# Performance work log

Hardware: AMD Instinct MI355X
Metric: run time of the kernel (lower is better)

The kernel has to match this reference:

```python
import jax, jax.numpy as jnp
import numpy as np

N_SPECIES = 4; N_BASIS = 128; N_GRAPH = 16; R_MAX = 6.0
NS_NODE, NV_NODE = 32, 16          # node irreps 32x0e + 16x1o
NS_EDGE = 16                       # initial edge irreps 16x0e
NS_OUT, NV_OUT = 16, 8             # output irreps 16x0e + 8x1o
NS_IN = 2 * NS_NODE + NS_EDGE      # 80 concatenated scalars
NV_IN = 2 * NV_NODE                # 32 concatenated vectors
NS_CONV = NS_OUT + NV_OUT          # 24 scalars (16 features + 8 gates)
W_SIZES = [NS_IN * NS_CONV, NS_IN * NV_OUT, NV_IN * NV_OUT, NV_IN * NS_CONV, NV_IN * NV_OUT]
N_NODES, N_EDGES = 8192, 65536
EPS = 1e-5


def gaussian_basis(d, stop, n):
    offsets = jnp.linspace(0.0, stop, n)
    coeff = -0.5 / (offsets[1] - offsets[0]) ** 2
    return jnp.exp(coeff * (d[:, None] - offsets[None, :]) ** 2)


def seg_mean(vals, seg, cnt):
    return jax.ops.segment_sum(vals, seg, num_segments=N_GRAPH) / cnt[:, None]


def setup_inputs():
    key = jax.random.key(0)
    ks = jax.random.split(key, 20)
    rn = lambda k, shape, scale: jax.random.normal(k, shape, jnp.float32) * scale
    inp = {}
    inp["node_fea"] = rn(ks[0], (N_NODES, NS_NODE + 3 * NV_NODE), 1.0)
    d = 0.5 + 5.0 * jax.random.uniform(ks[1], (N_EDGES,), jnp.float32)
    vec = jax.random.normal(ks[2], (N_EDGES, 3), jnp.float32)
    inp["edge_attr"] = jnp.concatenate([d[:, None], vec], axis=1)
    inp["edge_index"] = jax.random.randint(ks[3], (2, N_EDGES), 0, N_NODES)
    inp["x"] = jax.random.randint(ks[4], (N_NODES,), 0, N_SPECIES)
    inp["batch"] = jnp.sort(jax.random.randint(ks[5], (N_NODES,), 0, N_GRAPH))
    inp["w_rh"] = rn(ks[6], (N_BASIS, 64), N_BASIS ** -0.5); inp["b_rh"] = jnp.zeros((64,), jnp.float32)
    inp["w_ro"] = rn(ks[7], (64, sum(W_SIZES)), 64 ** -0.5); inp["b_ro"] = jnp.zeros((sum(W_SIZES),), jnp.float32)
    inp["w_pre"] = rn(ks[8], (NS_EDGE, NS_EDGE), NS_EDGE ** -0.5); inp["b_pre"] = jnp.zeros((NS_EDGE,), jnp.float32)
    inp["w_sc"] = rn(ks[9], (NS_EDGE, N_SPECIES ** 2, NS_OUT), 1.0)
    inp["w_post_s"] = rn(ks[10], (NS_OUT, NS_OUT), NS_OUT ** -0.5); inp["b_post_s"] = jnp.zeros((NS_OUT,), jnp.float32)
    inp["w_post_v"] = rn(ks[11], (NV_OUT, NV_OUT), NV_OUT ** -0.5)
    inp["ln_w_s"] = jnp.ones((NS_OUT,), jnp.float32); inp["ln_b_s"] = jnp.zeros((NS_OUT,), jnp.float32)
    inp["ln_w_v"] = jnp.ones((NV_OUT,), jnp.float32)
    inp["w_skip"] = rn(ks[12], (NS_EDGE, NS_OUT), NS_EDGE ** -0.5)
    inp["w_edge_s"] = rn(ks[13], (NS_OUT, NS_OUT), NS_OUT ** -0.5); inp["b_edge_s"] = jnp.zeros((NS_OUT,), jnp.float32)
    inp["w_edge_v"] = rn(ks[14], (NV_OUT, NV_OUT), NV_OUT ** -0.5)
    return inp


def _forward(node_fea, edge_attr, w_rh, b_rh, w_ro, b_ro, w_pre, b_pre, w_sc,
             w_post_s, b_post_s, w_post_v, ln_w_s, ln_b_s, ln_w_v,
             w_skip, w_edge_s, b_edge_s, w_edge_v, edge_index, x, batch):
    E = edge_index.shape[1]
    idx_i, idx_j = edge_index[0], edge_index[1]
    one_hot = jax.nn.one_hot(N_SPECIES * x[idx_i] + x[idx_j], N_SPECIES ** 2, dtype=node_fea.dtype)
    d, vec = edge_attr[:, 0], edge_attr[:, 1:4]
    u = vec / (jnp.linalg.norm(vec, axis=1, keepdims=True) + 1e-12)
    Y1 = np.sqrt(3.0) * u                                   # l=1 sph harm, component norm; Y0 == 1
    rbf = gaussian_basis(d, R_MAX, N_BASIS)                 # edge_length_embedded
    edge_s0 = gaussian_basis(d, 6.0, NS_EDGE)               # distance_expansion -> initial edge scalars
    # self connection: edge scalars x species-pair one-hot -> output scalars
    sc = jnp.einsum('ei,ej,ijo->eo', edge_s0, one_hot, w_sc) / np.sqrt(NS_EDGE * N_SPECIES ** 2)
    edge_s = edge_s0 @ w_pre + b_pre                        # lin_pre
    # gather node features by edge indices and concat
    nf_i, nf_j = node_fea[idx_i], node_fea[idx_j]
    s_in = jnp.concatenate([nf_i[:, :NS_NODE], nf_j[:, :NS_NODE], edge_s], axis=1)  # [E,80]
    v_in = jnp.concatenate([nf_i[:, NS_NODE:].reshape(E, NV_NODE, 3),
                            nf_j[:, NS_NODE:].reshape(E, NV_NODE, 3)], axis=1)      # [E,32,3]
    # radial MLP -> per-edge tensor-product path weights
    h = jax.nn.silu(rbf @ w_rh + b_rh)
    w_all = h @ w_ro + b_ro                                 # [E, 3840]
    w1, w2, w3, w4, w5 = jnp.split(w_all, np.cumsum(W_SIZES)[:-1].tolist(), axis=1)
    # equivariant tensor-product paths (explicit l<=1 Clebsch-Gordan structure)
    s0 = jnp.einsum('ei,eio->eo', s_in, w1.reshape(E, NS_IN, NS_CONV)) / np.sqrt(NS_IN)            # 0e x 0e -> 0e
    vA = jnp.einsum('ei,eio,ec->eoc', s_in, w2.reshape(E, NS_IN, NV_OUT), Y1) / np.sqrt(NS_IN)     # 0e x 1o -> 1o
    vB = jnp.einsum('eic,eio->eoc', v_in, w3.reshape(E, NV_IN, NV_OUT)) / np.sqrt(NV_IN)           # 1o x 0e -> 1o
    s1 = jnp.einsum('eic,eio,ec->eo', v_in, w4.reshape(E, NV_IN, NS_CONV), Y1) / np.sqrt(3.0 * NV_IN)  # 1o.1o -> 0e
    vC = jnp.einsum('eic,eio->eoc', jnp.cross(v_in, Y1[:, None, :]), w5.reshape(E, NV_IN, NV_OUT)) / np.sqrt(2.0 * NV_IN)  # 1o x 1o -> 1o
    s_conv = s0 + s1                                        # [E,24]
    v_conv = vA + vB + vC                                   # [E,8,3]
    # gate nonlinearity inside conv
    s_out = jax.nn.silu(s_conv[:, :NS_OUT])
    v_out = v_conv * jax.nn.sigmoid(s_conv[:, NS_OUT:])[:, :, None]
    # lin_post then self connection
    s_out = s_out @ w_post_s + b_post_s + sc
    v_out = jnp.einsum('eic,io->eoc', v_out, w_post_v)
    # e3LayerNorm keyed by graph id of source node
    eb = batch[idx_i]
    cnt = jnp.maximum(jax.ops.segment_sum(jnp.ones((E,), s_out.dtype), eb, num_segments=N_GRAPH), 1.0)
    mu = seg_mean(s_out, eb, cnt)
    s_c = s_out - mu[eb]
    rms_s = jnp.sqrt(seg_mean(s_c ** 2, eb, cnt).mean(axis=1, keepdims=True) + EPS)
    s_n = s_c / rms_s[eb] * ln_w_s + ln_b_s
    rms_v = jnp.sqrt((seg_mean((v_out ** 2).sum(-1), eb, cnt) / 3.0).mean(axis=1, keepdims=True) + EPS)
    v_n = v_out / rms_v[eb][:, :, None] * ln_w_v[None, :, None]
    # skip connection from old edge features (scalars only)
    s_n = s_n + edge_s0 @ w_skip
    # final lin_edge
    s_fin = s_n @ w_edge_s + b_edge_s
    v_fin = jnp.einsum('eic,io->eoc', v_n, w_edge_v)
    return jnp.concatenate([s_fin, v_fin.reshape(E, NV_OUT * 3)], axis=1)  # [E,40]


def reference(node_fea, edge_attr, edge_index, x, batch, w_rh, b_rh, w_ro, b_ro,
              w_pre, b_pre, w_sc, w_post_s, b_post_s, w_post_v, ln_w_s, ln_b_s, ln_w_v,
              w_skip, w_edge_s, b_edge_s, w_edge_v):
    return _forward(node_fea, edge_attr, w_rh, b_rh, w_ro, b_ro, w_pre, b_pre, w_sc,
                    w_post_s, b_post_s, w_post_v, ln_w_s, ln_b_s, ln_w_v,
                    w_skip, w_edge_s, b_edge_s, w_edge_v, edge_index, x, batch)
```

## Files before the change

### kernel.cpp

```cpp
#include <hip/hip_runtime.h>

typedef unsigned short u16;
typedef unsigned int u32;
typedef __attribute__((ext_vector_type(8))) short short8;
typedef __attribute__((ext_vector_type(4))) float floatx4;

#define E_TOTAL 65536

__device__ __forceinline__ u16 f2bf(float f) {
    union { float f; u32 i; } c; c.f = f;
    const u32 u = c.i;
    const u32 r = (u + 0x7fffu + ((u >> 16) & 1u)) >> 16;
    return (u16)r;
}
__device__ __forceinline__ float bfu2f(u16 u) {
    union { u32 i; float f; } c; c.i = ((u32)u) << 16; return c.f;
}
__device__ __forceinline__ void split2(float x0, float x1, u32& hp, u32& lp) {
    union { float f; u32 u; } a0, a1, h0, h1, l0, l1;
    a0.f = x0; a1.f = x1;
    h0.u = a0.u & 0xFFFF0000u; h1.u = a1.u & 0xFFFF0000u;
    hp = __builtin_amdgcn_perm(a1.u, a0.u, 0x07060302u);
    l0.f = x0 - h0.f; l1.f = x1 - h1.f;
    lp = __builtin_amdgcn_perm(l1.u, l0.u, 0x07060302u);
}
union Frag8 { u32 u[4]; short8 s; };


__global__ void k_zero(float* __restrict__ ws) {
    const int i = threadIdx.x + blockIdx.x * blockDim.x;
    if (i < 1056) ws[i] = 0.0f;
}

__global__ __launch_bounds__(64) void k_probe(int* __restrict__ binv) {
    const int lane = threadIdx.x;
    const int q = lane >> 4;
    if (lane < 32) binv[lane] = lane;
    short8 bfr;
    #pragma unroll
    for (int j = 0; j < 8; ++j) bfr[j] = (short)f2bf((float)(q*8 + j + 1));
    #pragma unroll
    for (int s = 0; s < 32; ++s) {
        const int qa = s >> 3, ja = s & 7;
        short8 afr = {0,0,0,0,0,0,0,0};
        if (q == qa) afr[ja] = (short)f2bf(1.0f);
        floatx4 dc = {0.0f, 0.0f, 0.0f, 0.0f};
        dc = __builtin_amdgcn_mfma_f32_16x16x32_bf16(afr, bfr, dc, 0, 0, 0);
        if (lane == 0) {
            const int sB = (int)(dc[0] + 0.5f) - 1;
            if (sB >= 0 && sB < 32) binv[sB] = s;
        }
    }
}

__global__ __launch_bounds__(256) void k_edge_heavy(
    const float* __restrict__ node_fea, const float* __restrict__ edge_attr,
    const int* __restrict__ edge_index, const int* __restrict__ xsp,
    const float* __restrict__ w_rh, const float* __restrict__ b_rh,
    const float* __restrict__ w_ro, const float* __restrict__ b_ro,
    const float* __restrict__ w_pre, const float* __restrict__ b_pre,
    const float* __restrict__ w_sc, const float* __restrict__ w_post_s,
    const float* __restrict__ b_post_s, const float* __restrict__ w_post_v,
    const int* __restrict__ binv,
    float* __restrict__ out)
{
    __shared__ __align__(16) u16 a_rbf[2][16 * 128];
    __shared__ __align__(16) u16 a_h[2][16 * 64];
    __shared__ __align__(16) float sh_wt[16][258];
    __shared__ float sh_sin[16][80];
    __shared__ float sh_vl[16][3][32];
    __shared__ float sh_q[16][32];
    __shared__ float sh_cr[16][3][32];
    __shared__ float sh_acc[16][56];
    __shared__ float sh_es0[16][16];
    __shared__ float sh_y1[16][4];
    __shared__ int   sh_kmap[32];

    const int tid = threadIdx.x;
    const int ed = tid >> 4, l16 = tid & 15;
    const int lane = tid & 63, w = tid >> 6;
    const int quad = lane >> 4, l15 = lane & 15;
    const int e = blockIdx.x * 16 + ed;

    if (tid < 32) sh_kmap[tid] = binv[tid];

    const int ni = edge_index[e];
    const int nj = edge_index[E_TOTAL + e];
    const float4 ea = *(const float4*)(edge_attr + 4*e);
    const float d  = ea.x;
    const float vx = ea.y, vy = ea.z, vz = ea.w;
    const float invn = 1.0f / (sqrtf(vx*vx + vy*vy + vz*vz) + 1e-12f);
    const float Y0 = 1.7320508075688772f * vx * invn;
    const float Y1 = 1.7320508075688772f * vy * invn;
    const float Y2 = 1.7320508075688772f * vz * invn;
    if (l16 == 0) { sh_y1[ed][0] = Y0; sh_y1[ed][1] = Y1; sh_y1[ed][2] = Y2; }

    const float C128 = -0.5f * (127.0f/6.0f) * (127.0f/6.0f);
    const float S128 = 6.0f/127.0f;
    {
        short8 thi, tlo;
        #pragma unroll
        for (int r = 0; r < 8; ++r) {
            const int b = l16*8 + r;
            const float t = d - S128 * (float)b;
            const float x = expf(C128 * t * t);
            const u16 hi = f2bf(x);
            thi[r] = (short)hi;
            tlo[r] = (short)f2bf(x - bfu2f(hi));
        }
        *(short8*)&a_rbf[0][(l16*16 + ed)*8] = thi;
        *(short8*)&a_rbf[1][(l16*16 + ed)*8] = tlo;
    }
    {
        const float t = d - 0.4f * (float)l16;
        sh_es0[ed][l16] = expf(-3.125f * t * t);
    }

    const float rs80 = 0.11180339887498949f;
    const float rs32 = 0.17677669529663689f;
    {
        const float* fi = node_fea + (size_t)ni * 80;
        const float* fj = node_fea + (size_t)nj * 80;
        sh_sin[ed][2*l16+0]    = fi[2*l16+0] * rs80;
        sh_sin[ed][2*l16+1]    = fi[2*l16+1] * rs80;
        sh_sin[ed][32+2*l16+0] = fj[2*l16+0] * rs80;
        sh_sin[ed][32+2*l16+1] = fj[2*l16+1] * rs80;
        #pragma unroll
        for (int c = 0; c < 3; ++c) {
            sh_vl[ed][c][l16]      = fi[32 + 3*l16 + c] * rs32;
            sh_vl[ed][c][16 + l16] = fj[32 + 3*l16 + c] * rs32;
        }
    }
    for (int s = tid; s < 16*56; s += 256) (&sh_acc[0][0])[s] = 0.0f;
    __syncthreads();

    int km[8];
    u32 voff0[8], voff1[8];
    #pragma unroll
    for (int j = 0; j < 8; ++j) {
        km[j] = sh_kmap[quad*8 + j];
        voff0[j] = (u32)(km[j] * 3840 + l15);
        voff1[j] = voff0[j] + 32u * 3840u;
    }

    float my_sc;
    {
        const int o = l16;
        float es = b_pre[o];
        float sc = 0.0f;
        const int p = 4*xsp[ni] + xsp[nj];
        #pragma unroll
        for (int i = 0; i < 16; ++i) {
            const float g = sh_es0[ed][i];
            es += g * w_pre[i*16 + o];
            sc += g * w_sc[(i*16 + p)*16 + o];
        }
        sh_sin[ed][64 + o] = es * rs80;
        my_sc = sc * 0.0625f;
    }
    #pragma unroll
    for (int rr = 0; rr < 2; ++rr) {
        const int i = l16 + 16*rr;
        const float a0 = sh_vl[ed][0][i];
        const float a1 = sh_vl[ed][1][i];
        const float a2 = sh_vl[ed][2][i];
        sh_q[ed][i] = (a0*Y0 + a1*Y1 + a2*Y2) * 0.57735026918962573f;
        sh_cr[ed][0][i] = (a1*Y2 - a2*Y1) * 0.70710678118654746f;
        sh_cr[ed][1][i] = (a2*Y0 - a0*Y2) * 0.70710678118654746f;
        sh_cr[ed][2][i] = (a0*Y1 - a1*Y0) * 0.70710678118654746f;
    }

    {
        floatx4 hacc = {0.0f, 0.0f, 0.0f, 0.0f};
        #pragma unroll
        for (int kk = 0; kk < 4; ++kk) {
            const short8 ahi = *(const short8*)&a_rbf[0][((kk*4 + quad)*16 + l15)*8];
            const short8 alo = *(const short8*)&a_rbf[1][((kk*4 + quad)*16 + l15)*8];
            Frag8 bh, bl;
            #pragma unroll
            for (int jj = 0; jj < 4; ++jj) {
                const float x0 = w_rh[(size_t)(kk*32 + km[2*jj+0])*64 + w*16 + l15];
                const float x1 = w_rh[(size_t)(kk*32 + km[2*jj+1])*64 + w*16 + l15];
                split2(x0, x1, bh.u[jj], bl.u[jj]);
            }
            hacc = __builtin_amdgcn_mfma_f32_16x16x32_bf16(ahi, bh.s, hacc, 0, 0, 0);
            hacc = __builtin_amdgcn_mfma_f32_16x16x32_bf16(alo, bh.s, hacc, 0, 0, 0);
            hacc = __builtin_amdgcn_mfma_f32_16x16x32_bf16(ahi, bl.s, hacc, 0, 0, 0);
        }
        const int hn = w*16 + l15;
        const float bb = b_rh[hn];
        const int k8 = hn >> 3, j2 = hn & 7;
        #pragma unroll
        for (int r = 0; r < 4; ++r) {
            const float x = hacc[r] + bb;
            const float s = x / (1.0f + expf(-x));
            const int m = quad*4 + r;
            const u16 h = f2bf(s);
            a_h[0][(k8*16 + m)*8 + j2] = h;
            a_h[1][(k8*16 + m)*8 + j2] = f2bf(s - bfu2f(h));
        }
    }
    __syncthreads();

    const short8 a0h = *(const short8*)&a_h[0][((0*4 + quad)*16 + l15)*8];
    const short8 a1h = *(const short8*)&a_h[0][((1*4 + quad)*16 + l15)*8];
    const short8 a0l = *(const short8*)&a_h[1][((0*4 + quad)*16 + l15)*8];
    const short8 a1l = *(const short8*)&a_h[1][((1*4 + quad)*16 + l15)*8];

    for (int ch = 0; ch < 15; ++ch) {
        const int coff = ch * 256;
        floatx4 acc[4];
        float bias[4];
        #pragma unroll
        for (int ct = 0; ct < 4; ++ct) {
            const int sgct = __builtin_amdgcn_readfirstlane(ch*16 + w*4 + ct);
            const float* bp = w_ro + sgct*16;
            float f0[8], f1[8];
            #pragma unroll
            for (int j = 0; j < 8; ++j) {
                f0[j] = bp[voff0[j]];
                f1[j] = bp[voff1[j]];
            }
            Frag8 b0h, b0l, b1h, b1l;
            #pragma unroll
            for (int jj = 0; jj < 4; ++jj) {
                split2(f0[2*jj], f0[2*jj+1], b0h.u[jj], b0l.u[jj]);
                split2(f1[2*jj], f1[2*jj+1], b1h.u[jj], b1l.u[jj]);
            }
            floatx4 a = {0.0f, 0.0f, 0.0f, 0.0f};
            a = __builtin_amdgcn_mfma_f32_16x16x32_bf16(a0h, b0h.s, a, 0, 0, 0);
            a = __builtin_amdgcn_mfma_f32_16x16x32_bf16(a1h, b1h.s, a, 0, 0, 0);
            a = __builtin_amdgcn_mfma_f32_16x16x32_bf16(a0l, b0h.s, a, 0, 0, 0);
            a = __builtin_amdgcn_mfma_f32_16x16x32_bf16(a1l, b1h.s, a, 0, 0, 0);
            a = __builtin_amdgcn_mfma_f32_16x16x32_bf16(a0h, b0l.s, a, 0, 0, 0);
            a = __builtin_amdgcn_mfma_f32_16x16x32_bf16(a1h, b1l.s, a, 0, 0, 0);
            acc[ct] = a;
            bias[ct] = b_ro[sgct*16 + l15];
        }
        __syncthreads();
        #pragma unroll
        for (int ct = 0; ct < 4; ++ct) {
            const int col = w*64 + ct*16 + l15;
            #pragma unroll
            for (int r = 0; r < 4; ++r)
                sh_wt[quad*4 + r][col] = acc[ct][r] + bias[ct];
        }
        __syncthreads();

        if (ch <= 7) {
            const int hi = (ch == 7) ? 1920 : (coff + 256);
            for (int idx = tid; idx < 384; idx += 256) {
                const int eo = idx / 24, o = idx % 24;
                const int i0 = (coff > o) ? (coff - o + 23) / 24 : 0;
                int i1 = (hi - o + 23) / 24; if (i1 > 80) i1 = 80;
                float a = 0.0f;
                for (int i = i0; i < i1; ++i)
                    a += sh_sin[eo][i] * sh_wt[eo][i*24 + o - coff];
                sh_acc[eo][o] += a;
            }
        }
        if (ch == 7) {
            for (int idx = tid; idx < 128; idx += 256) {
                const int eo = idx >> 3, o = idx & 7;
                float a = 0.0f;
                #pragma unroll
                for (int i = 0; i < 16; ++i)
                    a += sh_sin[eo][i] * sh_wt[eo][128 + i*8 + o];
                sh_acc[eo][24 + o] += a;
            }
        }
        if (ch == 8 || ch == 9) {
            const int ib = (ch == 8) ? 16 : 48;
            for (int idx = tid; idx < 128; idx += 256) {
                const int eo = idx >> 3, o = idx & 7;
                float a = 0.0f;
                #pragma unroll
                for (int i2 = 0; i2 < 32; ++i2)
                    a += sh_sin[eo][ib + i2] * sh_wt[eo][i2*8 + o];
                sh_acc[eo][24 + o] += a;
            }
        }
        if (ch == 10) {
            for (int idx = tid; idx < 384; idx += 256) {
                const int eo = idx / 24, rem = idx % 24;
                const int o = rem / 3, cc = rem % 3;
                float a = 0.0f;
                #pragma unroll
                for (int i = 0; i < 32; ++i)
                    a += sh_vl[eo][cc][i] * sh_wt[eo][i*8 + o];
                sh_acc[eo][32 + o*3 + cc] += a;
            }
        }
        if (ch >= 11 && ch <= 13) {
            const int rel = coff - 2816;
            for (int idx = tid; idx < 384; idx += 256) {
                const int eo = idx / 24, o = idx % 24;
                const int i0 = (rel > o) ? (rel - o + 23) / 24 : 0;
                int i1 = (rel + 256 - o + 23) / 24; if (i1 > 32) i1 = 32;
                float a = 0.0f;
                for (int i = i0; i < i1; ++i)
                    a += sh_q[eo][i] * sh_wt[eo][i*24 + o - rel];
                sh_acc[eo][o] += a;
            }
        }
        if (ch == 14) {
            for (int idx = tid; idx < 384; idx += 256) {
                const int eo = idx / 24, rem = idx % 24;
                const int o = rem / 3, cc = rem % 3;
                float a = 0.0f;
                #pragma unroll
                for (int i = 0; i < 32; ++i)
                    a += sh_cr[eo][cc][i] * sh_wt[eo][i*8 + o];
                sh_acc[eo][32 + o*3 + cc] += a;
            }
        }
    }
    __syncthreads();

    {
        const int o = l16;
        float a = b_post_s[o] + my_sc;
        #pragma unroll
        for (int i = 0; i < 16; ++i) {
            const float sv = sh_acc[ed][i];
            a += (sv / (1.0f + expf(-sv))) * w_post_s[i*16 + o];
        }
        out[(size_t)e*40 + o] = a;
    }
    if (l16 < 8) {
        const int o = l16;
        const float Ya = sh_y1[ed][0], Yb = sh_y1[ed][1], Yc = sh_y1[ed][2];
        float r0 = 0.0f, r1 = 0.0f, r2 = 0.0f;
        #pragma unroll
        for (int i = 0; i < 8; ++i) {
            const float g  = 1.0f / (1.0f + expf(-sh_acc[ed][16 + i]));
            const float a2 = sh_acc[ed][24 + i];
            const float ww = w_post_v[i*8 + o];
            r0 += (a2*Ya + sh_acc[ed][32 + i*3 + 0]) * g * ww;
            r1 += (a2*Yb + sh_acc[ed][32 + i*3 + 1]) * g * ww;
            r2 += (a2*Yc + sh_acc[ed][32 + i*3 + 2]) * g * ww;
        }
        out[(size_t)e*40 + 16 + o*3 + 0] = r0;
        out[(size_t)e*40 + 16 + o*3 + 1] = r1;
        out[(size_t)e*40 + 16 + o*3 + 2] = r2;
    }
}

__global__ __launch_bounds__(256) void k_stats_partial(
    const float* __restrict__ sv, const int* __restrict__ edge_index,
    const int* __restrict__ batch, float* __restrict__ ws)
{
    __shared__ float sh_ed[256][40];
    __shared__ int   sh_eb[256];
    const int tid = threadIdx.x;
    const int e = blockIdx.x * 256 + tid;
    sh_eb[tid] = batch[edge_index[e]];
    const float* p = sv + (size_t)e * 40;
    #pragma unroll
    for (int j = 0; j < 40; ++j) sh_ed[tid][j] = p[j];
    __syncthreads();

    for (int slot = tid; slot < 768; slot += 256) {
        const int g = slot / 48, s = slot % 48;
        float acc = 0.0f;
        if (s < 16) {
            for (int k = 0; k < 256; ++k) {
                const float m = (sh_eb[k] == g) ? 1.0f : 0.0f;
                acc += m * sh_ed[k][s];
            }
        } else if (s < 32) {
            for (int k = 0; k < 256; ++k) {
                const float m = (sh_eb[k] == g) ? 1.0f : 0.0f;
                const float v = sh_ed[k][s - 16];
                acc += m * v * v;
            }
        } else if (s < 40) {
            const int o3 = 16 + (s - 32) * 3;
            for (int k = 0; k < 256; ++k) {
                const float m = (sh_eb[k] == g) ? 1.0f : 0.0f;
                const float v0 = sh_ed[k][o3], v1 = sh_ed[k][o3+1], v2 = sh_ed[k][o3+2];
                acc += m * (v0*v0 + v1*v1 + v2*v2);
            }
        } else if (s == 40) {
            for (int k = 0; k < 256; ++k) acc += (sh_eb[k] == g) ? 1.0f : 0.0f;
        }
        atomicAdd(&ws[slot], acc);
    }
}

__global__ __launch_bounds__(64) void k_stats_final(float* __restrict__ ws)
{
    const int tid = threadIdx.x;
    if (tid < 16) {
        const int g = tid;
        float cnt = ws[g*48 + 40]; if (cnt < 1.0f) cnt = 1.0f;
        const float ic = 1.0f / cnt;
        float vs = 0.0f;
        for (int chn = 0; chn < 16; ++chn) {
            const float mu = ws[g*48 + chn] * ic;
            ws[768 + g*16 + chn] = mu;
            vs += ws[g*48 + 16 + chn] * ic - mu * mu;
        }
        if (vs < 0.0f) vs = 0.0f;
        ws[1024 + g] = 1.0f / sqrtf(vs * (1.0f/16.0f) + 1e-5f);
        float vv = 0.0f;
        for (int o = 0; o < 8; ++o) vv += ws[g*48 + 32 + o];
        vv = vv * ic * (1.0f/3.0f) * (1.0f/8.0f);
        ws[1040 + g] = 1.0f / sqrtf(vv + 1e-5f);
    }
}

__global__ __launch_bounds__(256) void k_edge_final(
    float* buf, const float* __restrict__ ws,
    const float* __restrict__ edge_attr, const int* __restrict__ edge_index,
    const int* __restrict__ batch,
    const float* __restrict__ ln_w_s, const float* __restrict__ ln_b_s,
    const float* __restrict__ ln_w_v, const float* __restrict__ w_skip,
    const float* __restrict__ w_edge_s, const float* __restrict__ b_edge_s,
    const float* __restrict__ w_edge_v)
{
    __shared__ float sh_mu[16][16];
    __shared__ float sh_is[16], sh_iv[16];
    __shared__ float sh_lws[16], sh_lbs[16], sh_lwv[8];
    __shared__ float sh_skip[16][16], sh_wes[16][16], sh_bes[16], sh_wev[8][8];
    const int tid = threadIdx.x;
    sh_mu[tid >> 4][tid & 15]   = ws[768 + tid];
    sh_skip[tid >> 4][tid & 15] = w_skip[tid];
    sh_wes[tid >> 4][tid & 15]  = w_edge_s[tid];
    if (tid < 16) {
        sh_is[tid]  = ws[1024 + tid];
        sh_iv[tid]  = ws[1040 + tid];
        sh_lws[tid] = ln_w_s[tid];
        sh_lbs[tid] = ln_b_s[tid];
        sh_bes[tid] = b_edge_s[tid];
    }
    if (tid < 8)  sh_lwv[tid] = ln_w_v[tid];
    if (tid < 64) sh_wev[tid >> 3][tid & 7] = w_edge_v[tid];
    __syncthreads();

    const int e = blockIdx.x * 256 + tid;
    const int g = batch[edge_index[e]];
    const float d = edge_attr[4*e];
    float es0[16];
    #pragma unroll
    for (int b = 0; b < 16; ++b) {
        const float t = d - 0.4f * (float)b;
        es0[b] = expf(-3.125f * t * t);
    }
    float p[40];
    float* pb = buf + (size_t)e * 40;
    #pragma unroll
    for (int j = 0; j < 40; ++j) p[j] = pb[j];

    const float is = sh_is[g];
    float sn[16];
    #pragma unroll
    for (int chn = 0; chn < 16; ++chn)
        sn[chn] = (p[chn] - sh_mu[g][chn]) * is * sh_lws[chn] + sh_lbs[chn];
    #pragma unroll
    for (int b = 0; b < 16; ++b) {
        const float g0 = es0[b];
        #pragma unroll
        for (int chn = 0; chn < 16; ++chn) sn[chn] += g0 * sh_skip[b][chn];
    }
    #pragma unroll
    for (int o = 0; o < 16; ++o) {
        float a = sh_bes[o];
        #pragma unroll
        for (int chn = 0; chn < 16; ++chn) a += sn[chn] * sh_wes[chn][o];
        pb[o] = a;
    }
    const float iv = sh_iv[g];
    float vn[8][3];
    #pragma unroll
    for (int i = 0; i < 8; ++i) {
        const float f = iv * sh_lwv[i];
        vn[i][0] = p[16 + i*3 + 0] * f;
        vn[i][1] = p[16 + i*3 + 1] * f;
        vn[i][2] = p[16 + i*3 + 2] * f;
    }
    #pragma unroll
    for (int o = 0; o < 8; ++o) {
        float r0 = 0.0f, r1 = 0.0f, r2 = 0.0f;
        #pragma unroll
        for (int i = 0; i < 8; ++i) {
            const float w = sh_wev[i][o];
            r0 += vn[i][0] * w; r1 += vn[i][1] * w; r2 += vn[i][2] * w;
        }
        pb[16 + o*3 + 0] = r0;
        pb[16 + o*3 + 1] = r1;
        pb[16 + o*3 + 2] = r2;
    }
}

extern "C" void kernel_launch(void* const* d_in, const int* in_sizes, int n_in,
                              void* d_out, int out_size, void* d_ws, size_t ws_size,
                              hipStream_t stream)
{
    const float* node_fea  = (const float*)d_in[0];
    const float* edge_attr = (const float*)d_in[1];
    const int* edge_index  = (const int*)d_in[2];
    const int* xsp         = (const int*)d_in[3];
    const int* batch       = (const int*)d_in[4];
    const float* w_rh      = (const float*)d_in[5];
    const float* b_rh      = (const float*)d_in[6];
    const float* w_ro      = (const float*)d_in[7];
    const float* b_ro      = (const float*)d_in[8];
    const float* w_pre     = (const float*)d_in[9];
    const float* b_pre     = (const float*)d_in[10];
    const float* w_sc      = (const float*)d_in[11];
    const float* w_post_s  = (const float*)d_in[12];
    const float* b_post_s  = (const float*)d_in[13];
    const float* w_post_v  = (const float*)d_in[14];
    const float* ln_w_s    = (const float*)d_in[15];
    const float* ln_b_s    = (const float*)d_in[16];
    const float* ln_w_v    = (const float*)d_in[17];
    const float* w_skip    = (const float*)d_in[18];
    const float* w_edge_s  = (const float*)d_in[19];
    const float* b_edge_s  = (const float*)d_in[20];
    const float* w_edge_v  = (const float*)d_in[21];

    float* ws   = (float*)d_ws;
    int*   binv = (int*)(ws + 1056);
    float* out  = (float*)d_out;

    k_zero<<<2, 1024, 0, stream>>>(ws);
    k_probe<<<1, 64, 0, stream>>>(binv);
    k_edge_heavy<<<4096, 256, 0, stream>>>(node_fea, edge_attr, edge_index, xsp,
        w_rh, b_rh, w_ro, b_ro, w_pre, b_pre, w_sc, w_post_s, b_post_s, w_post_v,
        binv, out);
    k_stats_partial<<<256, 256, 0, stream>>>(out, edge_index, batch, ws);
    k_stats_final<<<1, 64, 0, stream>>>(ws);
    k_edge_final<<<256, 256, 0, stream>>>(out, ws, edge_attr, edge_index,
        batch, ln_w_s, ln_b_s, ln_w_v, w_skip, w_edge_s, b_edge_s, w_edge_v);
}
```

Before: 483.8 us.

## Process 32 edges per block to reuse split weight fragments across two MFMA groups

The heavy edge kernel now handles two 16-edge groups per block, so each loaded and bf16-split readout weight fragment feeds MFMAs for both groups. This halves global weight traffic and split work per edge. Chunk width drops to 128 columns so the per-edge weight tile still fits in a shared pool that is reused for the RBF and hidden activations. The q and cross-product precomputation is folded into the contraction loops. It also merges the zero and probe kernels into one launch and pads a shared array to avoid bank conflicts. The cost is more shared memory and registers per block, which may lower occupancy, plus twice as many chunk iterations and barriers.

```diff
diff --git a/kernel.cpp b/kernel.cpp
--- a/kernel.cpp
+++ b/kernel.cpp
@@ -27,13 +27,9 @@
 union Frag8 { u32 u[4]; short8 s; };
 
 
-__global__ void k_zero(float* __restrict__ ws) {
-    const int i = threadIdx.x + blockIdx.x * blockDim.x;
-    if (i < 1056) ws[i] = 0.0f;
-}
-
-__global__ __launch_bounds__(64) void k_probe(int* __restrict__ binv) {
+__global__ __launch_bounds__(64) void k_init(float* __restrict__ ws, int* __restrict__ binv) {
     const int lane = threadIdx.x;
+    for (int i = lane; i < 1056; i += 64) ws[i] = 0.0f;
     const int q = lane >> 4;
     if (lane < 32) binv[lane] = lane;
     short8 bfr;
@@ -64,74 +60,79 @@
     const int* __restrict__ binv,
     float* __restrict__ out)
 {
-    __shared__ __align__(16) u16 a_rbf[2][16 * 128];
-    __shared__ __align__(16) u16 a_h[2][16 * 64];
-    __shared__ __align__(16) float sh_wt[16][258];
-    __shared__ float sh_sin[16][80];
-    __shared__ float sh_vl[16][3][32];
-    __shared__ float sh_q[16][32];
-    __shared__ float sh_cr[16][3][32];
-    __shared__ float sh_acc[16][56];
-    __shared__ float sh_es0[16][16];
-    __shared__ float sh_y1[16][4];
+    __shared__ __align__(16) char pool[32 * 129 * 4];
+    __shared__ float sh_sin[32][81];
+    __shared__ float sh_vl[32][3][32];
+    __shared__ float sh_acc[32][56];
+    __shared__ float sh_es0[32][16];
+    __shared__ float sh_y1[32][4];
     __shared__ int   sh_kmap[32];
+
+    u16* pool16 = (u16*)pool;
+    float (*sh_wt)[129] = (float(*)[129])pool;
 
     const int tid = threadIdx.x;
     const int ed = tid >> 4, l16 = tid & 15;
     const int lane = tid & 63, w = tid >> 6;
     const int quad = lane >> 4, l15 = lane & 15;
-    const int e = blockIdx.x * 16 + ed;
 
     if (tid < 32) sh_kmap[tid] = binv[tid];
-
-    const int ni = edge_index[e];
-    const int nj = edge_index[E_TOTAL + e];
-    const float4 ea = *(const float4*)(edge_attr + 4*e);
-    const float d  = ea.x;
-    const float vx = ea.y, vy = ea.z, vz = ea.w;
-    const float invn = 1.0f / (sqrtf(vx*vx + vy*vy + vz*vz) + 1e-12f);
-    const float Y0 = 1.7320508075688772f * vx * invn;
-    const float Y1 = 1.7320508075688772f * vy * invn;
-    const float Y2 = 1.7320508075688772f * vz * invn;
-    if (l16 == 0) { sh_y1[ed][0] = Y0; sh_y1[ed][1] = Y1; sh_y1[ed][2] = Y2; }
 
     const float C128 = -0.5f * (127.0f/6.0f) * (127.0f/6.0f);
     const float S128 = 6.0f/127.0f;
-    {
-        short8 thi, tlo;
-        #pragma unroll
-        for (int r = 0; r < 8; ++r) {
-            const int b = l16*8 + r;
-            const float t = d - S128 * (float)b;
-            const float x = expf(C128 * t * t);
-            const u16 hi = f2bf(x);
-            thi[r] = (short)hi;
-            tlo[r] = (short)f2bf(x - bfu2f(hi));
-        }
-        *(short8*)&a_rbf[0][(l16*16 + ed)*8] = thi;
-        *(short8*)&a_rbf[1][(l16*16 + ed)*8] = tlo;
-    }
-    {
-        const float t = d - 0.4f * (float)l16;
-        sh_es0[ed][l16] = expf(-3.125f * t * t);
-    }
-
     const float rs80 = 0.11180339887498949f;
     const float rs32 = 0.17677669529663689f;
-    {
-        const float* fi = node_fea + (size_t)ni * 80;
-        const float* fj = node_fea + (size_t)nj * 80;
-        sh_sin[ed][2*l16+0]    = fi[2*l16+0] * rs80;
-        sh_sin[ed][2*l16+1]    = fi[2*l16+1] * rs80;
-        sh_sin[ed][32+2*l16+0] = fj[2*l16+0] * rs80;
-        sh_sin[ed][32+2*l16+1] = fj[2*l16+1] * rs80;
-        #pragma unroll
-        for (int c = 0; c < 3; ++c) {
-            sh_vl[ed][c][l16]      = fi[32 + 3*l16 + c] * rs32;
-            sh_vl[ed][c][16 + l16] = fj[32 + 3*l16 + c] * rs32;
-        }
-    }
-    for (int s = tid; s < 16*56; s += 256) (&sh_acc[0][0])[s] = 0.0f;
+
+    int pp[2];
+    #pragma unroll
+    for (int g = 0; g < 2; ++g) {
+        const int e  = blockIdx.x * 32 + g*16 + ed;
+        const int ge = g*16 + ed;
+        const int ni = edge_index[e];
+        const int nj = edge_index[E_TOTAL + e];
+        pp[g] = 4*xsp[ni] + xsp[nj];
+        const float4 ea = *(const float4*)(edge_attr + 4*e);
+        const float d  = ea.x;
+        const float vx = ea.y, vy = ea.z, vz = ea.w;
+        const float invn = 1.0f / (sqrtf(vx*vx + vy*vy + vz*vz) + 1e-12f);
+        if (l16 == 0) {
+            sh_y1[ge][0] = 1.7320508075688772f * vx * invn;
+            sh_y1[ge][1] = 1.7320508075688772f * vy * invn;
+            sh_y1[ge][2] = 1.7320508075688772f * vz * invn;
+        }
+        {
+            short8 thi, tlo;
+            #pragma unroll
+            for (int r = 0; r < 8; ++r) {
+                const int b = l16*8 + r;
+                const float t = d - S128 * (float)b;
+                const float x = expf(C128 * t * t);
+                const u16 hi = f2bf(x);
+                thi[r] = (short)hi;
+                tlo[r] = (short)f2bf(x - bfu2f(hi));
+            }
+            *(short8*)&pool16[(0*2 + g)*2048 + (l16*16 + ed)*8] = thi;
+            *(short8*)&pool16[(1*2 + g)*2048 + (l16*16 + ed)*8] = tlo;
+        }
+        {
+            const float t = d - 0.4f * (float)l16;
+            sh_es0[ge][l16] = expf(-3.125f * t * t);
+        }
+        {
+            const float* fi = node_fea + (size_t)ni * 80;
+            const float* fj = node_fea + (size_t)nj * 80;
+            sh_sin[ge][2*l16+0]    = fi[2*l16+0] * rs80;
+            sh_sin[ge][2*l16+1]    = fi[2*l16+1] * rs80;
+            sh_sin[ge][32+2*l16+0] = fj[2*l16+0] * rs80;
+            sh_sin[ge][32+2*l16+1] = fj[2*l16+1] * rs80;
+            #pragma unroll
+            for (int c = 0; c < 3; ++c) {
+                sh_vl[ge][c][l16]      = fi[32 + 3*l16 + c] * rs32;
+                sh_vl[ge][c][16 + l16] = fj[32 + 3*l16 + c] * rs32;
+            }
+        }
+    }
+    for (int s = tid; s < 32*56; s += 256) (&sh_acc[0][0])[s] = 0.0f;
     __syncthreads();
 
     int km[8];
@@ -143,77 +144,78 @@
         voff1[j] = voff0[j] + 32u * 3840u;
     }
 
-    float my_sc;
-    {
+    float my_sc[2];
+    #pragma unroll
+    for (int g = 0; g < 2; ++g) {
+        const int ge = g*16 + ed;
         const int o = l16;
         float es = b_pre[o];
         float sc = 0.0f;
-        const int p = 4*xsp[ni] + xsp[nj];
+        const int p = pp[g];
         #pragma unroll
         for (int i = 0; i < 16; ++i) {
-            const float g = sh_es0[ed][i];
-            es += g * w_pre[i*16 + o];
-            sc += g * w_sc[(i*16 + p)*16 + o];
-        }
-        sh_sin[ed][64 + o] = es * rs80;
-        my_sc = sc * 0.0625f;
-    }
-    #pragma unroll
-    for (int rr = 0; rr < 2; ++rr) {
-        const int i = l16 + 16*rr;
-        const float a0 = sh_vl[ed][0][i];
-        const float a1 = sh_vl[ed][1][i];
-        const float a2 = sh_vl[ed][2][i];
-        sh_q[ed][i] = (a0*Y0 + a1*Y1 + a2*Y2) * 0.57735026918962573f;
-        sh_cr[ed][0][i] = (a1*Y2 - a2*Y1) * 0.70710678118654746f;
-        sh_cr[ed][1][i] = (a2*Y0 - a0*Y2) * 0.70710678118654746f;
-        sh_cr[ed][2][i] = (a0*Y1 - a1*Y0) * 0.70710678118654746f;
-    }
-
+            const float gg = sh_es0[ge][i];
+            es += gg * w_pre[i*16 + o];
+            sc += gg * w_sc[(i*16 + p)*16 + o];
+        }
+        sh_sin[ge][64 + o] = es * rs80;
+        my_sc[g] = sc * 0.0625f;
+    }
+
+    floatx4 hacc[2] = {{0,0,0,0},{0,0,0,0}};
+    #pragma unroll
+    for (int kk = 0; kk < 4; ++kk) {
+        Frag8 bh, bl;
+        #pragma unroll
+        for (int jj = 0; jj < 4; ++jj) {
+            const float x0 = w_rh[(size_t)(kk*32 + km[2*jj+0])*64 + w*16 + l15];
+            const float x1 = w_rh[(size_t)(kk*32 + km[2*jj+1])*64 + w*16 + l15];
+            split2(x0, x1, bh.u[jj], bl.u[jj]);
+        }
+        #pragma unroll
+        for (int g = 0; g < 2; ++g) {
+            const short8 ahi = *(const short8*)&pool16[(0*2 + g)*2048 + ((kk*4 + quad)*16 + l15)*8];
+            const short8 alo = *(const short8*)&pool16[(1*2 + g)*2048 + ((kk*4 + quad)*16 + l15)*8];
+            hacc[g] = __builtin_amdgcn_mfma_f32_16x16x32_bf16(ahi, bh.s, hacc[g], 0, 0, 0);
+            hacc[g] = __builtin_amdgcn_mfma_f32_16x16x32_bf16(alo, bh.s, hacc[g], 0, 0, 0);
+            hacc[g] = __builtin_amdgcn_mfma_f32_16x16x32_bf16(ahi, bl.s, hacc[g], 0, 0, 0);
+        }
+    }
+    __syncthreads();
     {
-        floatx4 hacc = {0.0f, 0.0f, 0.0f, 0.0f};
-        #pragma unroll
-        for (int kk = 0; kk < 4; ++kk) {
-            const short8 ahi = *(const short8*)&a_rbf[0][((kk*4 + quad)*16 + l15)*8];
-            const short8 alo = *(const short8*)&a_rbf[1][((kk*4 + quad)*16 + l15)*8];
-            Frag8 bh, bl;
-            #pragma unroll
-            for (int jj = 0; jj < 4; ++jj) {
-                const float x0 = w_rh[(size_t)(kk*32 + km[2*jj+0])*64 + w*16 + l15];
-                const float x1 = w_rh[(size_t)(kk*32 + km[2*jj+1])*64 + w*16 + l15];
-                split2(x0, x1, bh.u[jj], bl.u[jj]);
-            }
-            hacc = __builtin_amdgcn_mfma_f32_16x16x32_bf16(ahi, bh.s, hacc, 0, 0, 0);
-            hacc = __builtin_amdgcn_mfma_f32_16x16x32_bf16(alo, bh.s, hacc, 0, 0, 0);
-            hacc = __builtin_amdgcn_mfma_f32_16x16x32_bf16(ahi, bl.s, hacc, 0, 0, 0);
-        }
         const int hn = w*16 + l15;
         const float bb = b_rh[hn];
         const int k8 = hn >> 3, j2 = hn & 7;
         #pragma unroll
-        for (int r = 0; r < 4; ++r) {
-            const float x = hacc[r] + bb;
-            const float s = x / (1.0f + expf(-x));
-            const int m = quad*4 + r;
-            const u16 h = f2bf(s);
-            a_h[0][(k8*16 + m)*8 + j2] = h;
-            a_h[1][(k8*16 + m)*8 + j2] = f2bf(s - bfu2f(h));
+        for (int g = 0; g < 2; ++g) {
+            #pragma unroll
+            for (int r = 0; r < 4; ++r) {
+                const float x = hacc[g][r] + bb;
+                const float s = x / (1.0f + expf(-x));
+                const int m = quad*4 + r;
+                const u16 h = f2bf(s);
+                pool16[(0*2 + g)*1024 + (k8*16 + m)*8 + j2] = h;
+                pool16[(1*2 + g)*1024 + (k8*16 + m)*8 + j2] = f2bf(s - bfu2f(h));
+            }
         }
     }
     __syncthreads();
-
-    const short8 a0h = *(const short8*)&a_h[0][((0*4 + quad)*16 + l15)*8];
-    const short8 a1h = *(const short8*)&a_h[0][((1*4 + quad)*16 + l15)*8];
-    const short8 a0l = *(const short8*)&a_h[1][((0*4 + quad)*16 + l15)*8];
-    const short8 a1l = *(const short8*)&a_h[1][((1*4 + quad)*16 + l15)*8];
-
-    for (int ch = 0; ch < 15; ++ch) {
-        const int coff = ch * 256;
-        floatx4 acc[4];
-        float bias[4];
-        #pragma unroll
-        for (int ct = 0; ct < 4; ++ct) {
-            const int sgct = __builtin_amdgcn_readfirstlane(ch*16 + w*4 + ct);
+    short8 ah_[2][2], al_[2][2];
+    #pragma unroll
+    for (int f = 0; f < 2; ++f)
+        #pragma unroll
+        for (int g = 0; g < 2; ++g) {
+            ah_[f][g] = *(const short8*)&pool16[(0*2 + g)*1024 + ((f*4 + quad)*16 + l15)*8];
+            al_[f][g] = *(const short8*)&pool16[(1*2 + g)*1024 + ((f*4 + quad)*16 + l15)*8];
+        }
+
+    for (int ch = 0; ch < 30; ++ch) {
+        const int coff = ch * 128;
+        floatx4 acc[2][2];
+        float bias[2];
+        #pragma unroll
+        for (int ct = 0; ct < 2; ++ct) {
+            const int sgct = __builtin_amdgcn_readfirstlane(ch*8 + w*2 + ct);
             const float* bp = w_ro + sgct*16;
             float f0[8], f1[8];
             #pragma unroll
@@ -227,122 +229,126 @@
                 split2(f0[2*jj], f0[2*jj+1], b0h.u[jj], b0l.u[jj]);
                 split2(f1[2*jj], f1[2*jj+1], b1h.u[jj], b1l.u[jj]);
             }
-            floatx4 a = {0.0f, 0.0f, 0.0f, 0.0f};
-            a = __builtin_amdgcn_mfma_f32_16x16x32_bf16(a0h, b0h.s, a, 0, 0, 0);
-            a = __builtin_amdgcn_mfma_f32_16x16x32_bf16(a1h, b1h.s, a, 0, 0, 0);
-            a = __builtin_amdgcn_mfma_f32_16x16x32_bf16(a0l, b0h.s, a, 0, 0, 0);
-            a = __builtin_amdgcn_mfma_f32_16x16x32_bf16(a1l, b1h.s, a, 0, 0, 0);
-            a = __builtin_amdgcn_mfma_f32_16x16x32_bf16(a0h, b0l.s, a, 0, 0, 0);
-            a = __builtin_amdgcn_mfma_f32_16x16x32_bf16(a1h, b1l.s, a, 0, 0, 0);
-            acc[ct] = a;
+            #pragma unroll
+            for (int g = 0; g < 2; ++g) {
+                floatx4 a = {0.0f, 0.0f, 0.0f, 0.0f};
+                a = __builtin_amdgcn_mfma_f32_16x16x32_bf16(ah_[0][g], b0h.s, a, 0, 0, 0);
+                a = __builtin_amdgcn_mfma_f32_16x16x32_bf16(ah_[1][g], b1h.s, a, 0, 0, 0);
+                a = __builtin_amdgcn_mfma_f32_16x16x32_bf16(al_[0][g], b0h.s, a, 0, 0, 0);
+                a = __builtin_amdgcn_mfma_f32_16x16x32_bf16(al_[1][g], b1h.s, a, 0, 0, 0);
+                a = __builtin_amdgcn_mfma_f32_16x16x32_bf16(ah_[0][g], b0l.s, a, 0, 0, 0);
+                a = __builtin_amdgcn_mfma_f32_16x16x32_bf16(ah_[1][g], b1l.s, a, 0, 0, 0);
+                acc[ct][g] = a;
+            }
             bias[ct] = b_ro[sgct*16 + l15];
         }
         __syncthreads();
         #pragma unroll
-        for (int ct = 0; ct < 4; ++ct) {
-            const int col = w*64 + ct*16 + l15;
-            #pragma unroll
-            for (int r = 0; r < 4; ++r)
-                sh_wt[quad*4 + r][col] = acc[ct][r] + bias[ct];
+        for (int ct = 0; ct < 2; ++ct) {
+            const int col = w*32 + ct*16 + l15;
+            #pragma unroll
+            for (int g = 0; g < 2; ++g)
+                #pragma unroll
+                for (int r = 0; r < 4; ++r)
+                    sh_wt[g*16 + quad*4 + r][col] = acc[ct][g][r] + bias[ct];
         }
         __syncthreads();
 
-        if (ch <= 7) {
-            const int hi = (ch == 7) ? 1920 : (coff + 256);
-            for (int idx = tid; idx < 384; idx += 256) {
+        if (ch < 15) {
+            for (int idx = tid; idx < 768; idx += 256) {
                 const int eo = idx / 24, o = idx % 24;
                 const int i0 = (coff > o) ? (coff - o + 23) / 24 : 0;
-                int i1 = (hi - o + 23) / 24; if (i1 > 80) i1 = 80;
+                int i1 = (coff + 128 - o + 23) / 24; if (i1 > 80) i1 = 80;
                 float a = 0.0f;
                 for (int i = i0; i < i1; ++i)
                     a += sh_sin[eo][i] * sh_wt[eo][i*24 + o - coff];
                 sh_acc[eo][o] += a;
             }
-        }
-        if (ch == 7) {
-            for (int idx = tid; idx < 128; idx += 256) {
-                const int eo = idx >> 3, o = idx & 7;
-                float a = 0.0f;
-                #pragma unroll
-                for (int i = 0; i < 16; ++i)
-                    a += sh_sin[eo][i] * sh_wt[eo][128 + i*8 + o];
-                sh_acc[eo][24 + o] += a;
-            }
-        }
-        if (ch == 8 || ch == 9) {
-            const int ib = (ch == 8) ? 16 : 48;
-            for (int idx = tid; idx < 128; idx += 256) {
-                const int eo = idx >> 3, o = idx & 7;
-                float a = 0.0f;
-                #pragma unroll
-                for (int i2 = 0; i2 < 32; ++i2)
-                    a += sh_sin[eo][ib + i2] * sh_wt[eo][i2*8 + o];
-                sh_acc[eo][24 + o] += a;
-            }
-        }
-        if (ch == 10) {
-            for (int idx = tid; idx < 384; idx += 256) {
+        } else if (ch < 20) {
+            const int ib = (ch - 15) * 16;
+            const int eo = tid >> 3, o = tid & 7;
+            float a = 0.0f;
+            #pragma unroll
+            for (int i = 0; i < 16; ++i)
+                a += sh_sin[eo][ib + i] * sh_wt[eo][i*8 + o];
+            sh_acc[eo][24 + o] += a;
+        } else if (ch < 22) {
+            const int ib = (ch - 20) * 16;
+            for (int idx = tid; idx < 768; idx += 256) {
                 const int eo = idx / 24, rem = idx % 24;
                 const int o = rem / 3, cc = rem % 3;
                 float a = 0.0f;
                 #pragma unroll
-                for (int i = 0; i < 32; ++i)
-                    a += sh_vl[eo][cc][i] * sh_wt[eo][i*8 + o];
+                for (int i = 0; i < 16; ++i)
+                    a += sh_vl[eo][cc][ib + i] * sh_wt[eo][i*8 + o];
                 sh_acc[eo][32 + o*3 + cc] += a;
             }
-        }
-        if (ch >= 11 && ch <= 13) {
+        } else if (ch < 28) {
             const int rel = coff - 2816;
-            for (int idx = tid; idx < 384; idx += 256) {
+            for (int idx = tid; idx < 768; idx += 256) {
                 const int eo = idx / 24, o = idx % 24;
                 const int i0 = (rel > o) ? (rel - o + 23) / 24 : 0;
-                int i1 = (rel + 256 - o + 23) / 24; if (i1 > 32) i1 = 32;
-                float a = 0.0f;
-                for (int i = i0; i < i1; ++i)
-                    a += sh_q[eo][i] * sh_wt[eo][i*24 + o - rel];
-                sh_acc[eo][o] += a;
-            }
-        }
-        if (ch == 14) {
-            for (int idx = tid; idx < 384; idx += 256) {
-                const int eo = idx / 24, rem = idx % 24;
-                const int o = rem / 3, cc = rem % 3;
-                float a = 0.0f;
-                #pragma unroll
-                for (int i = 0; i < 32; ++i)
-                    a += sh_cr[eo][cc][i] * sh_wt[eo][i*8 + o];
-                sh_acc[eo][32 + o*3 + cc] += a;
-            }
+                int i1 = (rel + 128 - o + 23) / 24; if (i1 > 32) i1 = 32;
+                float t0 = 0.0f, t1 = 0.0f, t2 = 0.0f;
+                for (int i = i0; i < i1; ++i) {
+                    const float wv = sh_wt[eo][i*24 + o - rel];
+                    t0 += sh_vl[eo][0][i] * wv;
+                    t1 += sh_vl[eo][1][i] * wv;
+                    t2 += sh_vl[eo][2][i] * wv;
+                }
+                sh_acc[eo][o] += (t0*sh_y1[eo][0] + t1*sh_y1[eo][1] + t2*sh_y1[eo][2])
+                                 * 0.57735026918962573f;
+            }
+        } else {
+            const int ib = (ch - 28) * 16;
+            const int eo = tid >> 3, o = tid & 7;
+            float t0 = 0.0f, t1 = 0.0f, t2 = 0.0f;
+            #pragma unroll
+            for (int i = 0; i < 16; ++i) {
+                const float wv = sh_wt[eo][i*8 + o];
+                t0 += sh_vl[eo][0][ib + i] * wv;
+                t1 += sh_vl[eo][1][ib + i] * wv;
+                t2 += sh_vl[eo][2][ib + i] * wv;
+            }
+            const float Ya = sh_y1[eo][0], Yb = sh_y1[eo][1], Yc = sh_y1[eo][2];
+            sh_acc[eo][32 + o*3 + 0] += 0.70710678118654746f * (t1*Yc - t2*Yb);
+            sh_acc[eo][32 + o*3 + 1] += 0.70710678118654746f * (t2*Ya - t0*Yc);
+            sh_acc[eo][32 + o*3 + 2] += 0.70710678118654746f * (t0*Yb - t1*Ya);
         }
     }
     __syncthreads();
 
-    {
-        const int o = l16;
-        float a = b_post_s[o] + my_sc;
-        #pragma unroll
-        for (int i = 0; i < 16; ++i) {
-            const float sv = sh_acc[ed][i];
-            a += (sv / (1.0f + expf(-sv))) * w_post_s[i*16 + o];
-        }
-        out[(size_t)e*40 + o] = a;
-    }
-    if (l16 < 8) {
-        const int o = l16;
-        const float Ya = sh_y1[ed][0], Yb = sh_y1[ed][1], Yc = sh_y1[ed][2];
-        float r0 = 0.0f, r1 = 0.0f, r2 = 0.0f;
-        #pragma unroll
-        for (int i = 0; i < 8; ++i) {
-            const float g  = 1.0f / (1.0f + expf(-sh_acc[ed][16 + i]));
-            const float a2 = sh_acc[ed][24 + i];
-            const float ww = w_post_v[i*8 + o];
-            r0 += (a2*Ya + sh_acc[ed][32 + i*3 + 0]) * g * ww;
-            r1 += (a2*Yb + sh_acc[ed][32 + i*3 + 1]) * g * ww;
-            r2 += (a2*Yc + sh_acc[ed][32 + i*3 + 2]) * g * ww;
-        }
-        out[(size_t)e*40 + 16 + o*3 + 0] = r0;
-        out[(size_t)e*40 + 16 + o*3 + 1] = r1;
-        out[(size_t)e*40 + 16 + o*3 + 2] = r2;
+    #pragma unroll
+    for (int g = 0; g < 2; ++g) {
+        const int e  = blockIdx.x * 32 + g*16 + ed;
+        const int ge = g*16 + ed;
+        {
+            const int o = l16;
+            float a = b_post_s[o] + my_sc[g];
+            #pragma unroll
+            for (int i = 0; i < 16; ++i) {
+                const float sv = sh_acc[ge][i];
+                a += (sv / (1.0f + expf(-sv))) * w_post_s[i*16 + o];
+            }
+            out[(size_t)e*40 + o] = a;
+        }
+        if (l16 < 8) {
+            const int o = l16;
+            const float Ya = sh_y1[ge][0], Yb = sh_y1[ge][1], Yc = sh_y1[ge][2];
+            float r0 = 0.0f, r1 = 0.0f, r2 = 0.0f;
+            #pragma unroll
+            for (int i = 0; i < 8; ++i) {
+                const float gg = 1.0f / (1.0f + expf(-sh_acc[ge][16 + i]));
+                const float a2 = sh_acc[ge][24 + i];
+                const float ww = w_post_v[i*8 + o];
+                r0 += (a2*Ya + sh_acc[ge][32 + i*3 + 0]) * gg * ww;
+                r1 += (a2*Yb + sh_acc[ge][32 + i*3 + 1]) * gg * ww;
+                r2 += (a2*Yc + sh_acc[ge][32 + i*3 + 2]) * gg * ww;
+            }
+            out[(size_t)e*40 + 16 + o*3 + 0] = r0;
+            out[(size_t)e*40 + 16 + o*3 + 1] = r1;
+            out[(size_t)e*40 + 16 + o*3 + 2] = r2;
+        }
     }
 }
 
@@ -350,7 +356,7 @@
     const float* __restrict__ sv, const int* __restrict__ edge_index,
     const int* __restrict__ batch, float* __restrict__ ws)
 {
-    __shared__ float sh_ed[256][40];
+    __shared__ float sh_ed[256][41];
     __shared__ int   sh_eb[256];
     const int tid = threadIdx.x;
     const int e = blockIdx.x * 256 + tid;
@@ -524,9 +530,8 @@
     int*   binv = (int*)(ws + 1056);
     float* out  = (float*)d_out;
 
-    k_zero<<<2, 1024, 0, stream>>>(ws);
-    k_probe<<<1, 64, 0, stream>>>(binv);
-    k_edge_heavy<<<4096, 256, 0, stream>>>(node_fea, edge_attr, edge_index, xsp,
+    k_init<<<1, 64, 0, stream>>>(ws, binv);
+    k_edge_heavy<<<2048, 256, 0, stream>>>(node_fea, edge_attr, edge_index, xsp,
         w_rh, b_rh, w_ro, b_ro, w_pre, b_pre, w_sc, w_post_s, b_post_s, w_post_v,
         binv, out);
     k_stats_partial<<<256, 256, 0, stream>>>(out, edge_index, batch, ws);
```

Measured after the change: 491.2 us. Within noise of the previous version (+1.5%).
